# Kernel tuning notes

Measured on AMD Instinct MI355X. Metric: run time of the kernel, lower is better.

## Reference

```python
import jax, jax.numpy as jnp
import numpy as np

B = 256        # graphs (documents) per batch
NPG = 200      # nodes per graph
EPG = 1600     # edges per graph (~2*ngram+2 per token)
D = 200        # hidden_size_node (glove.6B.200d)
V = 50000      # vocab size
ENUM = 2000000 # global edge-id vocabulary
C = 20         # class_num
N = B * NPG
E = B * EPG


def setup_inputs() -> dict:
    key = jax.random.key(0)
    ks = jax.random.split(key, 8)
    node_ids = jax.random.randint(ks[0], (N,), 0, V, dtype=jnp.int32)
    # graph-local endpoints + per-graph node offset (mimics dgl.batch)
    src_local = jax.random.randint(ks[1], (E,), 0, NPG, dtype=jnp.int32)
    dst_local = jax.random.randint(ks[2], (E,), 0, NPG, dtype=jnp.int32)
    off = jnp.repeat(jnp.arange(B, dtype=jnp.int32) * NPG, EPG)
    edge_src = src_local + off
    edge_dst = dst_local + off
    edge_ids = jax.random.randint(ks[3], (E,), 0, ENUM, dtype=jnp.int32)
    node_seg = jnp.repeat(jnp.arange(B, dtype=jnp.int32), NPG)
    node_emb = jax.random.normal(ks[4], (V, D), dtype=jnp.float32) * 0.1
    # trainable_edges=True -> edge weight table initialized to ones
    edge_w = jnp.ones((ENUM, 1), dtype=jnp.float32)
    W = jax.random.normal(ks[5], (D, C), dtype=jnp.float32) * 0.05
    b = jnp.zeros((C,), dtype=jnp.float32)
    return {"node_emb": node_emb, "edge_w": edge_w, "W": W, "b": b,
            "node_ids": node_ids, "edge_src": edge_src, "edge_dst": edge_dst,
            "edge_ids": edge_ids, "node_seg": node_seg}


def reference(node_emb, edge_w, W, b, node_ids, edge_src, edge_dst, edge_ids, node_seg):
    h = node_emb[node_ids]                       # [N, D] node hidden states
    msg = h[edge_src] * edge_w[edge_ids]         # [E, D] src feat * edge weight
    # scatter-max reduce onto destination nodes (dgl max reduce)
    h_max = jax.ops.segment_max(msg, edge_dst, num_segments=N)
    h_max = jnp.where(jnp.isfinite(h_max), h_max, jnp.float32(0.0))  # empty segs -> 0 like DGL
    pooled = jax.ops.segment_sum(h_max, node_seg, num_segments=B)   # dgl.sum_nodes -> [B, D]
    # dropout is identity in eval / p=0.0
    return jax.nn.relu(pooled) @ W + b           # [B, C]
```

## Files before the change

### kernel.cpp

```cpp
#include <hip/hip_runtime.h>

#define NPG 200
#define EPG 1600
#define DIM 200
#define NCLS 20
#define THREADS 1024
#define NWAVES 16
#define Q4 50
#define NEG_INF (-__builtin_inff())

__global__ __launch_bounds__(THREADS, 4) void gnn_fused(
    const float* __restrict__ node_emb,
    const float* __restrict__ edge_w,
    const float* __restrict__ Wm,
    const float* __restrict__ bv,
    const int*   __restrict__ node_ids,
    const int*   __restrict__ edge_src,
    const int*   __restrict__ edge_dst,
    const int*   __restrict__ edge_ids,
    float*       __restrict__ out)
{
    __shared__ int            nidrow[NPG];
    __shared__ unsigned short srcl[EPG];
    __shared__ unsigned short dstl[EPG];
    __shared__ float          wv[EPG];
    __shared__ uint2          ce[EPG];
    __shared__ int            csum[256];
    __shared__ int            cursor[NPG];
    __shared__ short          wstart[NWAVES + 1];
    __shared__ float          part[NWAVES][DIM];
    __shared__ float          pooled[DIM];

    const int g       = blockIdx.x;
    const int tid     = threadIdx.x;
    const int gbase_n = g * NPG;
    const int gbase_e = g * EPG;

    for (int n = tid; n < NPG; n += THREADS)
        nidrow[n] = node_ids[gbase_n + n] * DIM;

    if (tid < 256) csum[tid] = 0;
    __syncthreads();

    for (int e = tid; e < EPG; e += THREADS) {
        int s = edge_src[gbase_e + e] - gbase_n;
        int d = edge_dst[gbase_e + e] - gbase_n;
        srcl[e] = (unsigned short)s;
        dstl[e] = (unsigned short)d;
        wv[e]   = edge_w[edge_ids[gbase_e + e]];
        atomicAdd(&csum[d], 1);
    }
    __syncthreads();

    for (int off = 1; off < 256; off <<= 1) {
        int v = 0;
        if (tid < 256) {
            v = csum[tid];
            if (tid >= off) v += csum[tid - off];
        }
        __syncthreads();
        if (tid < 256) csum[tid] = v;
        __syncthreads();
    }
    if (tid < NPG) cursor[tid] = (tid == 0) ? 0 : csum[tid - 1];
    if (tid <= NWAVES) {
        int target = tid * (EPG / NWAVES);
        int lo = 0, hi = NPG;
        while (lo < hi) {
            int mid = (lo + hi) >> 1;
            int excl = (mid == 0) ? 0 : csum[mid - 1];
            if (excl >= target) hi = mid; else lo = mid + 1;
        }
        wstart[tid] = (short)lo;
    }
    __syncthreads();

    for (int e = tid; e < EPG; e += THREADS) {
        int d   = dstl[e];
        int pos = atomicAdd(&cursor[d], 1);
        unsigned pack = ((unsigned)nidrow[srcl[e]] << 8) | (unsigned)d;
        ce[pos] = make_uint2(pack, __float_as_uint(wv[e]));
    }
    __syncthreads();

    const int w    = tid >> 6;
    const int lane = tid & 63;
    if (lane < Q4) {
        const int n0 = wstart[w];
        const int n1 = wstart[w + 1];
        const int kb = (n0 == 0) ? 0 : csum[n0 - 1];
        const int ke = (n1 == 0) ? 0 : csum[n1 - 1];

        float4 p = make_float4(0.f, 0.f, 0.f, 0.f);
        float4 m = make_float4(NEG_INF, NEG_INF, NEG_INF, NEG_INF);
        int curn = (kb < ke) ? (int)(ce[kb].x & 255u) : -1;

        #pragma unroll 8
        for (int k = kb; k < ke; ++k) {
            const uint2 q2  = ce[k];
            const int   dn  = (int)(q2.x & 255u);
            const float wgt = __uint_as_float(q2.y);
            const float4 v  = *(reinterpret_cast<const float4*>(node_emb + (q2.x >> 8)) + lane);
            const bool  ns  = (dn != curn);
            p.x += ns ? m.x : 0.0f;
            p.y += ns ? m.y : 0.0f;
            p.z += ns ? m.z : 0.0f;
            p.w += ns ? m.w : 0.0f;
            m.x = ns ? NEG_INF : m.x;
            m.y = ns ? NEG_INF : m.y;
            m.z = ns ? NEG_INF : m.z;
            m.w = ns ? NEG_INF : m.w;
            curn = dn;
            m.x = fmaxf(m.x, v.x * wgt);
            m.y = fmaxf(m.y, v.y * wgt);
            m.z = fmaxf(m.z, v.z * wgt);
            m.w = fmaxf(m.w, v.w * wgt);
        }
        if (kb < ke) { p.x += m.x; p.y += m.y; p.z += m.z; p.w += m.w; }
        *reinterpret_cast<float4*>(&part[w][lane * 4]) = p;
    }
    __syncthreads();

    if (tid < DIM) {
        float t = 0.f;
        #pragma unroll
        for (int i = 0; i < NWAVES; ++i) t += part[i][tid];
        pooled[tid] = fmaxf(t, 0.0f);
    }
    __syncthreads();

    if (tid < NCLS) {
        float acc = bv[tid];
        #pragma unroll 4
        for (int k = 0; k < DIM; ++k)
            acc += pooled[k] * Wm[k * NCLS + tid];
        out[g * NCLS + tid] = acc;
    }
}

extern "C" void kernel_launch(void* const* d_in, const int* in_sizes, int n_in,
                              void* d_out, int out_size, void* d_ws, size_t ws_size,
                              hipStream_t stream) {
    const float* node_emb = (const float*)d_in[0];
    const float* edge_w   = (const float*)d_in[1];
    const float* Wm       = (const float*)d_in[2];
    const float* bv       = (const float*)d_in[3];
    const int*   node_ids = (const int*)d_in[4];
    const int*   edge_src = (const int*)d_in[5];
    const int*   edge_dst = (const int*)d_in[6];
    const int*   edge_ids = (const int*)d_in[7];

    const int N = in_sizes[4];
    const int B = N / NPG;

    gnn_fused<<<B, THREADS, 0, stream>>>(node_emb, edge_w, Wm, bv,
                                         node_ids, edge_src, edge_dst, edge_ids,
                                         (float*)d_out);
}
```

Measured before the change: 128.2 us.

## Double-buffer gather loads in segment-max loop and precompute segment-start flags

The edge loop is restructured into blocks of 8 with two register buffers, so the next block's embedding gathers are issued while the current block is processed. Segment boundaries are now marked by a start flag in the low bit of the packed byte offset, computed at scatter time, instead of comparing destination ids. The 256-entry prefix scan is replaced by a single-wave shuffle scan over int4 chunks, which cuts the number of block barriers. This raises register pressure (16 float4 plus 16 uint2 live values) under a 1024-thread launch bound, and it adds clamped speculative loads past the end of each wave's range.

```diff
diff --git a/kernel.cpp b/kernel.cpp
--- a/kernel.cpp
+++ b/kernel.cpp
@@ -7,6 +7,7 @@
 #define THREADS 1024
 #define NWAVES 16
 #define Q4 50
+#define P 8
 #define NEG_INF (-__builtin_inff())
 
 __global__ __launch_bounds__(THREADS, 4) void gnn_fused(
@@ -37,8 +38,7 @@
     const int gbase_e = g * EPG;
 
     for (int n = tid; n < NPG; n += THREADS)
-        nidrow[n] = node_ids[gbase_n + n] * DIM;
-
+        nidrow[n] = node_ids[gbase_n + n] * (DIM * 4);
     if (tid < 256) csum[tid] = 0;
     __syncthreads();
 
@@ -52,16 +52,21 @@
     }
     __syncthreads();
 
-    for (int off = 1; off < 256; off <<= 1) {
-        int v = 0;
-        if (tid < 256) {
-            v = csum[tid];
-            if (tid >= off) v += csum[tid - off];
-        }
-        __syncthreads();
-        if (tid < 256) csum[tid] = v;
-        __syncthreads();
-    }
+    if (tid < 64) {
+        int4 c = *reinterpret_cast<int4*>(&csum[tid * 4]);
+        int s1 = c.x + c.y, s2 = s1 + c.z, s3 = s2 + c.w;
+        int carry = s3;
+        #pragma unroll
+        for (int off = 1; off < 64; off <<= 1) {
+            int t = __shfl_up(carry, off);
+            if (tid >= off) carry += t;
+        }
+        const int base = carry - s3;
+        int4 o; o.x = base + c.x; o.y = base + s1; o.z = base + s2; o.w = base + s3;
+        *reinterpret_cast<int4*>(&csum[tid * 4]) = o;
+    }
+    __syncthreads();
+
     if (tid < NPG) cursor[tid] = (tid == 0) ? 0 : csum[tid - 1];
     if (tid <= NWAVES) {
         int target = tid * (EPG / NWAVES);
@@ -76,9 +81,10 @@
     __syncthreads();
 
     for (int e = tid; e < EPG; e += THREADS) {
-        int d   = dstl[e];
-        int pos = atomicAdd(&cursor[d], 1);
-        unsigned pack = ((unsigned)nidrow[srcl[e]] << 8) | (unsigned)d;
+        int d    = dstl[e];
+        int excl = (d == 0) ? 0 : csum[d - 1];
+        int pos  = atomicAdd(&cursor[d], 1);
+        unsigned pack = (unsigned)nidrow[srcl[e]] | (pos == excl ? 1u : 0u);
         ce[pos] = make_uint2(pack, __float_as_uint(wv[e]));
     }
     __syncthreads();
@@ -90,33 +96,75 @@
         const int n1 = wstart[w + 1];
         const int kb = (n0 == 0) ? 0 : csum[n0 - 1];
         const int ke = (n1 == 0) ? 0 : csum[n1 - 1];
+        const int count = ke - kb;
+        const char* lb = (const char*)node_emb + lane * 16;
 
         float4 p = make_float4(0.f, 0.f, 0.f, 0.f);
         float4 m = make_float4(NEG_INF, NEG_INF, NEG_INF, NEG_INF);
-        int curn = (kb < ke) ? (int)(ce[kb].x & 255u) : -1;
-
-        #pragma unroll 8
-        for (int k = kb; k < ke; ++k) {
-            const uint2 q2  = ce[k];
-            const int   dn  = (int)(q2.x & 255u);
-            const float wgt = __uint_as_float(q2.y);
-            const float4 v  = *(reinterpret_cast<const float4*>(node_emb + (q2.x >> 8)) + lane);
-            const bool  ns  = (dn != curn);
-            p.x += ns ? m.x : 0.0f;
-            p.y += ns ? m.y : 0.0f;
-            p.z += ns ? m.z : 0.0f;
-            p.w += ns ? m.w : 0.0f;
-            m.x = ns ? NEG_INF : m.x;
-            m.y = ns ? NEG_INF : m.y;
-            m.z = ns ? NEG_INF : m.z;
-            m.w = ns ? NEG_INF : m.w;
-            curn = dn;
-            m.x = fmaxf(m.x, v.x * wgt);
-            m.y = fmaxf(m.y, v.y * wgt);
-            m.z = fmaxf(m.z, v.z * wgt);
-            m.w = fmaxf(m.w, v.w * wgt);
-        }
-        if (kb < ke) { p.x += m.x; p.y += m.y; p.z += m.z; p.w += m.w; }
+        uint2 qA[P], qB[P];
+        float4 vA[P], vB[P];
+
+#define LOADB(Q, V, BASE) do {                                                   \
+        _Pragma("unroll")                                                        \
+        for (int j = 0; j < P; ++j) {                                            \
+            int idx = (BASE) + j; idx = idx < EPG ? idx : EPG - 1;               \
+            Q[j] = ce[idx];                                                      \
+        }                                                                        \
+        _Pragma("unroll")                                                        \
+        for (int j = 0; j < P; ++j)                                              \
+            V[j] = *reinterpret_cast<const float4*>(lb + (Q[j].x & ~1u));        \
+    } while (0)
+
+#define PROCB(Q, V) do {                                                         \
+        _Pragma("unroll")                                                        \
+        for (int j = 0; j < P; ++j) {                                            \
+            const bool  ns  = (Q[j].x & 1u);                                     \
+            const float wgt = __uint_as_float(Q[j].y);                           \
+            p.x += ns ? m.x : 0.0f; p.y += ns ? m.y : 0.0f;                      \
+            p.z += ns ? m.z : 0.0f; p.w += ns ? m.w : 0.0f;                      \
+            m.x = ns ? NEG_INF : m.x; m.y = ns ? NEG_INF : m.y;                  \
+            m.z = ns ? NEG_INF : m.z; m.w = ns ? NEG_INF : m.w;                  \
+            m.x = fmaxf(m.x, V[j].x * wgt); m.y = fmaxf(m.y, V[j].y * wgt);      \
+            m.z = fmaxf(m.z, V[j].z * wgt); m.w = fmaxf(m.w, V[j].w * wgt);      \
+        }                                                                        \
+    } while (0)
+
+#define PROCM(Q, V, LIM) do {                                                    \
+        _Pragma("unroll")                                                        \
+        for (int j = 0; j < P; ++j) {                                            \
+            const bool  ok  = j < (LIM);                                         \
+            const bool  ns  = ok && (Q[j].x & 1u);                               \
+            const float wgt = __uint_as_float(Q[j].y);                           \
+            p.x += ns ? m.x : 0.0f; p.y += ns ? m.y : 0.0f;                      \
+            p.z += ns ? m.z : 0.0f; p.w += ns ? m.w : 0.0f;                      \
+            m.x = ns ? NEG_INF : m.x; m.y = ns ? NEG_INF : m.y;                  \
+            m.z = ns ? NEG_INF : m.z; m.w = ns ? NEG_INF : m.w;                  \
+            const float c0 = V[j].x * wgt, c1 = V[j].y * wgt;                    \
+            const float c2 = V[j].z * wgt, c3 = V[j].w * wgt;                    \
+            m.x = ok ? fmaxf(m.x, c0) : m.x; m.y = ok ? fmaxf(m.y, c1) : m.y;    \
+            m.z = ok ? fmaxf(m.z, c2) : m.z; m.w = ok ? fmaxf(m.w, c3) : m.w;    \
+        }                                                                        \
+    } while (0)
+
+        LOADB(qA, vA, kb);
+        qA[0].x &= ~1u;
+        const int nfull = count >> 3;
+        const int vlim  = count & 7;
+        int b = 0;
+        for (; b + 2 <= nfull; b += 2) {
+            LOADB(qB, vB, kb + (b + 1) * P);
+            PROCB(qA, vA);
+            LOADB(qA, vA, kb + (b + 2) * P);
+            PROCB(qB, vB);
+        }
+        if (b < nfull) {
+            LOADB(qB, vB, kb + (b + 1) * P);
+            PROCB(qA, vA);
+            PROCM(qB, vB, vlim);
+        } else {
+            PROCM(qA, vA, vlim);
+        }
+        if (count > 0) { p.x += m.x; p.y += m.y; p.z += m.z; p.w += m.w; }
         *reinterpret_cast<float4*>(&part[w][lane * 4]) = p;
     }
     __syncthreads();
```

Result: no change. 130.1 us (+1.5%).

## Stage graph node rows in LDS as bf16 and gather from shared memory

Applied to the files above, without the earlier changes.

Each block now loads its graph's 200 embedding rows once, rounds them to bf16 and stores them in shared memory. The per-edge gather then reads from LDS instead of repeating global float4 loads for every edge, removing redundant global traffic. Segment boundaries are precomputed as a flag bit in the packed edge record, and the 256-entry prefix scan is replaced by a single-wave shuffle scan. The trade-off is about 80KB of extra LDS per block, which reduces occupancy, plus a loss of precision from rounding the embeddings to bf16.

```diff
diff --git a/kernel.cpp b/kernel.cpp
--- a/kernel.cpp
+++ b/kernel.cpp
@@ -7,6 +7,8 @@
 #define THREADS 1024
 #define NWAVES 16
 #define Q4 50
+#define NROWU 100
+#define NCHUNK (NPG * Q4)
 #define NEG_INF (-__builtin_inff())
 
 __global__ __launch_bounds__(THREADS, 4) void gnn_fused(
@@ -20,11 +22,12 @@
     const int*   __restrict__ edge_ids,
     float*       __restrict__ out)
 {
+    __shared__ unsigned       rows[NPG * NROWU];
+    __shared__ uint2          ce[EPG];
     __shared__ int            nidrow[NPG];
     __shared__ unsigned short srcl[EPG];
     __shared__ unsigned short dstl[EPG];
     __shared__ float          wv[EPG];
-    __shared__ uint2          ce[EPG];
     __shared__ int            csum[256];
     __shared__ int            cursor[NPG];
     __shared__ short          wstart[NWAVES + 1];
@@ -36,9 +39,7 @@
     const int gbase_n = g * NPG;
     const int gbase_e = g * EPG;
 
-    for (int n = tid; n < NPG; n += THREADS)
-        nidrow[n] = node_ids[gbase_n + n] * DIM;
-
+    if (tid < NPG) nidrow[tid] = node_ids[gbase_n + tid];
     if (tid < 256) csum[tid] = 0;
     __syncthreads();
 
@@ -50,18 +51,35 @@
         wv[e]   = edge_w[edge_ids[gbase_e + e]];
         atomicAdd(&csum[d], 1);
     }
+
+    for (int i = tid; i < NCHUNK; i += THREADS) {
+        const int row = i / Q4;
+        const int c   = i - row * Q4;
+        const float4 v = *reinterpret_cast<const float4*>(
+            node_emb + (size_t)nidrow[row] * DIM + c * 4);
+        const unsigned b0 = ((__float_as_uint(v.y) + 0x8000u) & 0xffff0000u) |
+                            ((__float_as_uint(v.x) + 0x8000u) >> 16);
+        const unsigned b1 = ((__float_as_uint(v.w) + 0x8000u) & 0xffff0000u) |
+                            ((__float_as_uint(v.z) + 0x8000u) >> 16);
+        *reinterpret_cast<uint2*>(&rows[row * NROWU + c * 2]) = make_uint2(b0, b1);
+    }
     __syncthreads();
 
-    for (int off = 1; off < 256; off <<= 1) {
-        int v = 0;
-        if (tid < 256) {
-            v = csum[tid];
-            if (tid >= off) v += csum[tid - off];
+    if (tid < 64) {
+        int4 cc = *reinterpret_cast<int4*>(&csum[tid * 4]);
+        int s1 = cc.x + cc.y, s2 = s1 + cc.z, s3 = s2 + cc.w;
+        int carry = s3;
+        #pragma unroll
+        for (int off = 1; off < 64; off <<= 1) {
+            int t = __shfl_up(carry, off);
+            if (tid >= off) carry += t;
         }
-        __syncthreads();
-        if (tid < 256) csum[tid] = v;
-        __syncthreads();
+        const int base = carry - s3;
+        int4 o; o.x = base + cc.x; o.y = base + s1; o.z = base + s2; o.w = base + s3;
+        *reinterpret_cast<int4*>(&csum[tid * 4]) = o;
     }
+    __syncthreads();
+
     if (tid < NPG) cursor[tid] = (tid == 0) ? 0 : csum[tid - 1];
     if (tid <= NWAVES) {
         int target = tid * (EPG / NWAVES);
@@ -76,9 +94,10 @@
     __syncthreads();
 
     for (int e = tid; e < EPG; e += THREADS) {
-        int d   = dstl[e];
-        int pos = atomicAdd(&cursor[d], 1);
-        unsigned pack = ((unsigned)nidrow[srcl[e]] << 8) | (unsigned)d;
+        int d    = dstl[e];
+        int excl = (d == 0) ? 0 : csum[d - 1];
+        int pos  = atomicAdd(&cursor[d], 1);
+        unsigned pack = (unsigned)srcl[e] * 200u | (pos == excl ? 1u : 0u);
         ce[pos] = make_uint2(pack, __float_as_uint(wv[e]));
     }
     __syncthreads();
@@ -90,33 +109,29 @@
         const int n1 = wstart[w + 1];
         const int kb = (n0 == 0) ? 0 : csum[n0 - 1];
         const int ke = (n1 == 0) ? 0 : csum[n1 - 1];
+        const int lane2 = lane * 2;
 
         float4 p = make_float4(0.f, 0.f, 0.f, 0.f);
-        float4 m = make_float4(NEG_INF, NEG_INF, NEG_INF, NEG_INF);
-        int curn = (kb < ke) ? (int)(ce[kb].x & 255u) : -1;
+        float4 m = make_float4(0.f, 0.f, 0.f, 0.f);
 
         #pragma unroll 8
         for (int k = kb; k < ke; ++k) {
             const uint2 q2  = ce[k];
-            const int   dn  = (int)(q2.x & 255u);
+            const bool  ns  = (q2.x & 1u);
             const float wgt = __uint_as_float(q2.y);
-            const float4 v  = *(reinterpret_cast<const float4*>(node_emb + (q2.x >> 8)) + lane);
-            const bool  ns  = (dn != curn);
-            p.x += ns ? m.x : 0.0f;
-            p.y += ns ? m.y : 0.0f;
-            p.z += ns ? m.z : 0.0f;
-            p.w += ns ? m.w : 0.0f;
-            m.x = ns ? NEG_INF : m.x;
-            m.y = ns ? NEG_INF : m.y;
-            m.z = ns ? NEG_INF : m.z;
-            m.w = ns ? NEG_INF : m.w;
-            curn = dn;
-            m.x = fmaxf(m.x, v.x * wgt);
-            m.y = fmaxf(m.y, v.y * wgt);
-            m.z = fmaxf(m.z, v.z * wgt);
-            m.w = fmaxf(m.w, v.w * wgt);
+            const uint2 rv  = *reinterpret_cast<const uint2*>(&rows[(q2.x >> 1) + lane2]);
+            const float c0 = __uint_as_float(rv.x << 16)         * wgt;
+            const float c1 = __uint_as_float(rv.x & 0xffff0000u) * wgt;
+            const float c2 = __uint_as_float(rv.y << 16)         * wgt;
+            const float c3 = __uint_as_float(rv.y & 0xffff0000u) * wgt;
+            p.x += ns ? m.x : 0.0f;  p.y += ns ? m.y : 0.0f;
+            p.z += ns ? m.z : 0.0f;  p.w += ns ? m.w : 0.0f;
+            m.x = fmaxf(ns ? NEG_INF : m.x, c0);
+            m.y = fmaxf(ns ? NEG_INF : m.y, c1);
+            m.z = fmaxf(ns ? NEG_INF : m.z, c2);
+            m.w = fmaxf(ns ? NEG_INF : m.w, c3);
         }
-        if (kb < ke) { p.x += m.x; p.y += m.y; p.z += m.z; p.w += m.w; }
+        p.x += m.x; p.y += m.y; p.z += m.z; p.w += m.w;
         *reinterpret_cast<float4*>(&part[w][lane * 4]) = p;
     }
     __syncthreads();
```

Measured after the change: 131.9 us. +2.9%, slower.
